# Performance work log

Hardware: AMD Instinct MI355X
Metric: run time of the kernel (lower is better)

## Reference

```python
import jax, jax.numpy as jnp
import numpy as np

NUM_NODES = 8192
IN_FEATURES = 1024
OUT_FEATURES = 512
NUM_EDGES = 262144  # avg degree 32


def setup_inputs() -> dict:
    key = jax.random.key(0)
    k_x, k_w, k_b, k_src, k_dst = jax.random.split(key, 5)
    x = jax.random.normal(k_x, (NUM_NODES, IN_FEATURES), dtype=jnp.float32)
    # torch nn.Linear layout: weight [out, in], bias [out]
    W = jax.random.normal(k_w, (OUT_FEATURES, IN_FEATURES), dtype=jnp.float32) * (1.0 / np.sqrt(IN_FEATURES))
    b = jax.random.normal(k_b, (OUT_FEATURES,), dtype=jnp.float32) * 0.01
    src = jax.random.randint(k_src, (NUM_EDGES,), 0, NUM_NODES, dtype=jnp.int64)
    dst = jax.random.randint(k_dst, (NUM_EDGES,), 0, NUM_NODES, dtype=jnp.int64)
    edge_index = jnp.stack([src, dst], axis=0)
    return {"x": x, "W": W, "b": b, "edge_index": edge_index, "num_nodes": NUM_NODES}


def reference(x, W, b, edge_index, num_nodes):
    # Faithful to the torch module: build dense adjacency from edge list
    # (duplicate edges collapse to 1.0 via assignment semantics),
    # linear, (dropout p=0 -> identity), dense adj @ hidden, relu.
    adj = jnp.zeros((num_nodes, num_nodes), dtype=x.dtype)
    adj = adj.at[edge_index[0], edge_index[1]].set(1.0)
    hidden = x @ W.T + b            # [N, out]
    support = adj @ hidden          # [N, out] aggregation over neighbors
    return jax.nn.relu(support)
```

## Files before the change

### kernel.cpp

```cpp
#include <hip/hip_runtime.h>

#define N_NODES 8192
#define IN_F    1024
#define OUT_F   512
#define N_EDGES 262144
#define STRIDE  96

#define HID_OFF     0u
#define XB_OFF      8388608u
#define WB_OFF      25165824u
#define DEG_OFF     26214400u
#define COL_OFF     26247168u
#define MAX_DEG     STRIDE

typedef short  bf16x8 __attribute__((ext_vector_type(8)));
typedef float  f32x4  __attribute__((ext_vector_type(4)));

__device__ __forceinline__ unsigned short f2bf(float f) {
    unsigned u = __float_as_uint(f);
    u += 0x7fffu + ((u >> 16) & 1u);
    return (unsigned short)(u >> 16);
}

__device__ __forceinline__ float bflo(unsigned u) { return __uint_as_float(u << 16); }
__device__ __forceinline__ float bfhi(unsigned u) { return __uint_as_float(u & 0xffff0000u); }

__device__ __forceinline__ void ld_lds16(const void* g, void* l) {
    __builtin_amdgcn_global_load_lds(
        (const __attribute__((address_space(1))) void*)g,
        (__attribute__((address_space(3))) void*)l, 16, 0, 0);
}

#define NX8 (N_NODES * IN_F / 8)
#define NW8 (OUT_F * IN_F / 8)
__global__ __launch_bounds__(256) void cvt_bf16_all(const float* __restrict__ x,
                                                    const float* __restrict__ w,
                                                    unsigned short* __restrict__ xb,
                                                    int* __restrict__ deg) {
    int i = blockIdx.x * blockDim.x + threadIdx.x;
    if (i < N_NODES) deg[i] = 0;
    if (i >= NX8 + NW8) return;
    const f32x4* p = (i < NX8) ? ((const f32x4*)x + (size_t)i * 2)
                               : ((const f32x4*)w + (size_t)(i - NX8) * 2);
    f32x4 v0 = __builtin_nontemporal_load(p);
    f32x4 v1 = __builtin_nontemporal_load(p + 1);
    uint4 o;
    o.x = (unsigned)f2bf(v0.x) | ((unsigned)f2bf(v0.y) << 16);
    o.y = (unsigned)f2bf(v0.z) | ((unsigned)f2bf(v0.w) << 16);
    o.z = (unsigned)f2bf(v1.x) | ((unsigned)f2bf(v1.y) << 16);
    o.w = (unsigned)f2bf(v1.z) | ((unsigned)f2bf(v1.w) << 16);
    *((uint4*)xb + i) = o;
}

__global__ __launch_bounds__(256, 6) void gemm_scatter(const unsigned short* __restrict__ Xb,
                                                       const unsigned short* __restrict__ Wb,
                                                       const float* __restrict__ bias,
                                                       unsigned short* __restrict__ H,
                                                       const int* __restrict__ src,
                                                       const int* __restrict__ dst,
                                                       int* __restrict__ deg,
                                                       int* __restrict__ col) {
    __shared__ unsigned short As[64 * 64];
    __shared__ unsigned short Bs[64 * 64];

    const int bid = blockIdx.x;
    const int tid = threadIdx.x;

    if (bid >= 1024) {
        int e = (bid - 1024) * 256 + tid;
        int s = src[e];
        int slot = atomicAdd(&deg[s], 1);
        if (slot < STRIDE) col[s * STRIDE + slot] = dst[e];
        return;
    }

    const int lane = tid & 63;
    const int wave = tid >> 6;
    const int row0 = (bid & 127) * 64;
    const int col0 = (bid >> 7) * 64;
    const int wm   = (wave & 1) * 32;
    const int wn   = (wave >> 1) * 32;
    const int fm   = lane & 15;
    const int fm7  = fm & 7;
    const int q    = lane >> 4;

    f32x4 acc[2][2];
#pragma unroll
    for (int i = 0; i < 2; ++i)
#pragma unroll
        for (int j = 0; j < 2; ++j) acc[i][j] = (f32x4)0.f;

    const int r0 = tid >> 3;
    const int kp = ((tid & 7) ^ (r0 & 7)) * 8;

    for (int k0 = 0; k0 < IN_F; k0 += 64) {
        ld_lds16(Xb + (size_t)(row0 + r0) * IN_F + k0 + kp,      As + tid * 8);
        ld_lds16(Xb + (size_t)(row0 + r0 + 32) * IN_F + k0 + kp, As + (tid + 256) * 8);
        ld_lds16(Wb + (size_t)(col0 + r0) * IN_F + k0 + kp,      Bs + tid * 8);
        ld_lds16(Wb + (size_t)(col0 + r0 + 32) * IN_F + k0 + kp, Bs + (tid + 256) * 8);
        __syncthreads();

#pragma unroll
        for (int s = 0; s < 2; ++s) {
            const int kq = s * 4 + q;
            bf16x8 a[2], b[2];
#pragma unroll
            for (int mi = 0; mi < 2; ++mi)
                a[mi] = *(const bf16x8*)&As[(((wm + mi * 16 + fm) << 3) + (kq ^ fm7)) << 3];
#pragma unroll
            for (int ni = 0; ni < 2; ++ni)
                b[ni] = *(const bf16x8*)&Bs[(((wn + ni * 16 + fm) << 3) + (kq ^ fm7)) << 3];
#pragma unroll
            for (int mi = 0; mi < 2; ++mi)
#pragma unroll
                for (int ni = 0; ni < 2; ++ni)
                    acc[mi][ni] = __builtin_amdgcn_mfma_f32_16x16x32_bf16(
                        a[mi], b[ni], acc[mi][ni], 0, 0, 0);
        }
        __syncthreads();
    }

    const int cm = (lane >> 4) * 4;
#pragma unroll
    for (int ni = 0; ni < 2; ++ni) {
        const int c = col0 + wn + ni * 16 + fm;
        const float bv = bias[c];
#pragma unroll
        for (int mi = 0; mi < 2; ++mi) {
#pragma unroll
            for (int r = 0; r < 4; ++r) {
                const int row = row0 + wm + mi * 16 + cm + r;
                H[(size_t)row * OUT_F + c] = f2bf(acc[mi][ni][r] + bv);
            }
        }
    }
}

__global__ __launch_bounds__(256) void aggregate(const unsigned short* __restrict__ H,
                                                 const int* __restrict__ dg,
                                                 const int* __restrict__ col,
                                                 float* __restrict__ out) {
    __shared__ int nbr[4][MAX_DEG];
    __shared__ int uniq[4][MAX_DEG];
    __shared__ int wcnt[4];
    const int wave = threadIdx.x >> 6;
    const int lane = threadIdx.x & 63;
    const int v    = blockIdx.x * 4 + wave;
    int d = dg[v];
    if (d > MAX_DEG) d = MAX_DEG;

    if (lane == 0) wcnt[wave] = 0;
    int id0 = -1, id1 = -1;
    if (lane < d)      { id0 = col[v * STRIDE + lane];      nbr[wave][lane]      = id0; }
    if (64 + lane < d) { id1 = col[v * STRIDE + 64 + lane]; nbr[wave][64 + lane] = id1; }
    __builtin_amdgcn_wave_barrier();

    bool k0 = (lane < d);
    const int lim0 = k0 ? lane : 0;
    for (int j = 0; j < lim0; ++j) k0 = k0 & (nbr[wave][j] != id0);
    bool k1 = (64 + lane < d);
    const int lim1 = k1 ? (64 + lane) : 0;
    for (int j = 0; j < lim1; ++j) k1 = k1 & (nbr[wave][j] != id1);
    if (k0) uniq[wave][atomicAdd(&wcnt[wave], 1)] = id0;
    if (k1) uniq[wave][atomicAdd(&wcnt[wave], 1)] = id1;
    __builtin_amdgcn_wave_barrier();
    const int n  = wcnt[wave];
    const int f0 = lane * 8;

    float a0=0,a1=0,a2=0,a3=0,a4=0,a5=0,a6=0,a7=0;
    int e = 0;
    for (; e + 4 <= n; e += 4) {
        const int i0 = uniq[wave][e], i1 = uniq[wave][e+1],
                  i2 = uniq[wave][e+2], i3 = uniq[wave][e+3];
        uint4 h0 = *(const uint4*)&H[(size_t)i0 * OUT_F + f0];
        uint4 h1 = *(const uint4*)&H[(size_t)i1 * OUT_F + f0];
        uint4 h2 = *(const uint4*)&H[(size_t)i2 * OUT_F + f0];
        uint4 h3 = *(const uint4*)&H[(size_t)i3 * OUT_F + f0];
        a0 += bflo(h0.x)+bflo(h1.x)+bflo(h2.x)+bflo(h3.x);
        a1 += bfhi(h0.x)+bfhi(h1.x)+bfhi(h2.x)+bfhi(h3.x);
        a2 += bflo(h0.y)+bflo(h1.y)+bflo(h2.y)+bflo(h3.y);
        a3 += bfhi(h0.y)+bfhi(h1.y)+bfhi(h2.y)+bfhi(h3.y);
        a4 += bflo(h0.z)+bflo(h1.z)+bflo(h2.z)+bflo(h3.z);
        a5 += bfhi(h0.z)+bfhi(h1.z)+bfhi(h2.z)+bfhi(h3.z);
        a6 += bflo(h0.w)+bflo(h1.w)+bflo(h2.w)+bflo(h3.w);
        a7 += bfhi(h0.w)+bfhi(h1.w)+bfhi(h2.w)+bfhi(h3.w);
    }
    for (; e < n; ++e) {
        uint4 h0 = *(const uint4*)&H[(size_t)uniq[wave][e] * OUT_F + f0];
        a0 += bflo(h0.x); a1 += bfhi(h0.x);
        a2 += bflo(h0.y); a3 += bfhi(h0.y);
        a4 += bflo(h0.z); a5 += bfhi(h0.z);
        a6 += bflo(h0.w); a7 += bfhi(h0.w);
    }
    f32x4 o0 = {fmaxf(a0,0.f), fmaxf(a1,0.f), fmaxf(a2,0.f), fmaxf(a3,0.f)};
    f32x4 o1 = {fmaxf(a4,0.f), fmaxf(a5,0.f), fmaxf(a6,0.f), fmaxf(a7,0.f)};
    __builtin_nontemporal_store(o0, (f32x4*)&out[(size_t)v * OUT_F + f0]);
    __builtin_nontemporal_store(o1, (f32x4*)&out[(size_t)v * OUT_F + f0 + 4]);
}

extern "C" void kernel_launch(void* const* d_in, const int* in_sizes, int n_in,
                              void* d_out, int out_size, void* d_ws, size_t ws_size,
                              hipStream_t stream) {
    const float* x  = (const float*)d_in[0];
    const float* W  = (const float*)d_in[1];
    const float* b  = (const float*)d_in[2];
    const int*   ei = (const int*)d_in[3];
    float* out = (float*)d_out;

    char* ws = (char*)d_ws;
    unsigned short* H   = (unsigned short*)(ws + HID_OFF);
    unsigned short* Xb  = (unsigned short*)(ws + XB_OFF);
    unsigned short* Wb  = (unsigned short*)(ws + WB_OFF);
    int*            deg = (int*)(ws + DEG_OFF);
    int*            col = (int*)(ws + COL_OFF);

    cvt_bf16_all<<<(NX8 + NW8 + 255) / 256, 256, 0, stream>>>(x, W, Xb, deg);

    gemm_scatter<<<2048, 256, 0, stream>>>(Xb, Wb, b, H, ei, ei + N_EDGES, deg, col);

    aggregate<<<N_NODES / 4, 256, 0, stream>>>(H, deg, col, out);
}
```

Before: 139.5 us.

## Double-buffer GEMM LDS with 128x64 tiles and unroll aggregation by eight

The GEMM tile grows from 64x64 to 128x64, cutting the grid to 512 GEMM blocks. Each wave now computes a 64x32 sub-tile, and the LDS stages are double-buffered so the next K-slice loads while MFMAs run on the current one. The aggregation loop gains an 8-way unrolled gather to keep more loads in flight. The trade-offs are more registers and LDS per block (launch bounds drop to 2) and fewer blocks, which may underfill the GPU.

```diff
diff --git a/kernel.cpp b/kernel.cpp
--- a/kernel.cpp
+++ b/kernel.cpp
@@ -52,7 +52,9 @@
     *((uint4*)xb + i) = o;
 }
 
-__global__ __launch_bounds__(256, 6) void gemm_scatter(const unsigned short* __restrict__ Xb,
+#define GEMM_BLOCKS 512
+
+__global__ __launch_bounds__(256, 2) void gemm_scatter(const unsigned short* __restrict__ Xb,
                                                        const unsigned short* __restrict__ Wb,
                                                        const float* __restrict__ bias,
                                                        unsigned short* __restrict__ H,
@@ -60,14 +62,14 @@
                                                        const int* __restrict__ dst,
                                                        int* __restrict__ deg,
                                                        int* __restrict__ col) {
-    __shared__ unsigned short As[64 * 64];
-    __shared__ unsigned short Bs[64 * 64];
+    __shared__ unsigned short As[2][128 * 64];
+    __shared__ unsigned short Bs[2][64 * 64];
 
     const int bid = blockIdx.x;
     const int tid = threadIdx.x;
 
-    if (bid >= 1024) {
-        int e = (bid - 1024) * 256 + tid;
+    if (bid >= GEMM_BLOCKS) {
+        int e = (bid - GEMM_BLOCKS) * 256 + tid;
         int s = src[e];
         int slot = atomicAdd(&deg[s], 1);
         if (slot < STRIDE) col[s * STRIDE + slot] = dst[e];
@@ -76,49 +78,64 @@
 
     const int lane = tid & 63;
     const int wave = tid >> 6;
-    const int row0 = (bid & 127) * 64;
-    const int col0 = (bid >> 7) * 64;
-    const int wm   = (wave & 1) * 32;
+    const int row0 = (bid & 63) * 128;
+    const int col0 = (bid >> 6) * 64;
+    const int wm   = (wave & 1) * 64;
     const int wn   = (wave >> 1) * 32;
     const int fm   = lane & 15;
     const int fm7  = fm & 7;
     const int q    = lane >> 4;
 
-    f32x4 acc[2][2];
-#pragma unroll
-    for (int i = 0; i < 2; ++i)
+    f32x4 acc[4][2];
+#pragma unroll
+    for (int i = 0; i < 4; ++i)
 #pragma unroll
         for (int j = 0; j < 2; ++j) acc[i][j] = (f32x4)0.f;
 
     const int r0 = tid >> 3;
     const int kp = ((tid & 7) ^ (r0 & 7)) * 8;
-
-    for (int k0 = 0; k0 < IN_F; k0 += 64) {
-        ld_lds16(Xb + (size_t)(row0 + r0) * IN_F + k0 + kp,      As + tid * 8);
-        ld_lds16(Xb + (size_t)(row0 + r0 + 32) * IN_F + k0 + kp, As + (tid + 256) * 8);
-        ld_lds16(Wb + (size_t)(col0 + r0) * IN_F + k0 + kp,      Bs + tid * 8);
-        ld_lds16(Wb + (size_t)(col0 + r0 + 32) * IN_F + k0 + kp, Bs + (tid + 256) * 8);
+    const unsigned short* Xbase = Xb + (size_t)(row0 + r0) * IN_F + kp;
+    const unsigned short* Wbase = Wb + (size_t)(col0 + r0) * IN_F + kp;
+
+#define STAGE(buf, k0) do {                                                   \
+    ld_lds16(Xbase            + (k0), &As[buf][tid * 8]);                     \
+    ld_lds16(Xbase + 32*IN_F  + (k0), &As[buf][(tid + 256) * 8]);             \
+    ld_lds16(Xbase + 64*IN_F  + (k0), &As[buf][(tid + 512) * 8]);             \
+    ld_lds16(Xbase + 96*IN_F  + (k0), &As[buf][(tid + 768) * 8]);             \
+    ld_lds16(Wbase            + (k0), &Bs[buf][tid * 8]);                     \
+    ld_lds16(Wbase + 32*IN_F  + (k0), &Bs[buf][(tid + 256) * 8]);             \
+} while (0)
+
+#define COMPUTE(buf) do {                                                     \
+    _Pragma("unroll")                                                         \
+    for (int s = 0; s < 2; ++s) {                                             \
+        const int kq = s * 4 + q;                                             \
+        bf16x8 a[4], b[2];                                                    \
+        _Pragma("unroll")                                                     \
+        for (int mi = 0; mi < 4; ++mi)                                        \
+            a[mi] = *(const bf16x8*)&As[buf][(((wm + mi*16 + fm) << 3) + (kq ^ fm7)) << 3]; \
+        _Pragma("unroll")                                                     \
+        for (int ni = 0; ni < 2; ++ni)                                        \
+            b[ni] = *(const bf16x8*)&Bs[buf][(((wn + ni*16 + fm) << 3) + (kq ^ fm7)) << 3]; \
+        _Pragma("unroll")                                                     \
+        for (int mi = 0; mi < 4; ++mi)                                        \
+            _Pragma("unroll")                                                 \
+            for (int ni = 0; ni < 2; ++ni)                                    \
+                acc[mi][ni] = __builtin_amdgcn_mfma_f32_16x16x32_bf16(        \
+                    a[mi], b[ni], acc[mi][ni], 0, 0, 0);                      \
+    }                                                                         \
+} while (0)
+
+    STAGE(0, 0);
+    __syncthreads();
+    int cur = 0;
+    for (int t = 0; t < 15; ++t) {
+        STAGE(cur ^ 1, (t + 1) * 64);
+        COMPUTE(cur);
         __syncthreads();
-
-#pragma unroll
-        for (int s = 0; s < 2; ++s) {
-            const int kq = s * 4 + q;
-            bf16x8 a[2], b[2];
-#pragma unroll
-            for (int mi = 0; mi < 2; ++mi)
-                a[mi] = *(const bf16x8*)&As[(((wm + mi * 16 + fm) << 3) + (kq ^ fm7)) << 3];
-#pragma unroll
-            for (int ni = 0; ni < 2; ++ni)
-                b[ni] = *(const bf16x8*)&Bs[(((wn + ni * 16 + fm) << 3) + (kq ^ fm7)) << 3];
-#pragma unroll
-            for (int mi = 0; mi < 2; ++mi)
-#pragma unroll
-                for (int ni = 0; ni < 2; ++ni)
-                    acc[mi][ni] = __builtin_amdgcn_mfma_f32_16x16x32_bf16(
-                        a[mi], b[ni], acc[mi][ni], 0, 0, 0);
-        }
-        __syncthreads();
-    }
+        cur ^= 1;
+    }
+    COMPUTE(cur);
 
     const int cm = (lane >> 4) * 4;
 #pragma unroll
@@ -126,7 +143,7 @@
         const int c = col0 + wn + ni * 16 + fm;
         const float bv = bias[c];
 #pragma unroll
-        for (int mi = 0; mi < 2; ++mi) {
+        for (int mi = 0; mi < 4; ++mi) {
 #pragma unroll
             for (int r = 0; r < 4; ++r) {
                 const int row = row0 + wm + mi * 16 + cm + r;
@@ -134,6 +151,8 @@
             }
         }
     }
+#undef STAGE
+#undef COMPUTE
 }
 
 __global__ __launch_bounds__(256) void aggregate(const unsigned short* __restrict__ H,
@@ -169,6 +188,36 @@
 
     float a0=0,a1=0,a2=0,a3=0,a4=0,a5=0,a6=0,a7=0;
     int e = 0;
+    for (; e + 8 <= n; e += 8) {
+        const int i0 = uniq[wave][e],   i1 = uniq[wave][e+1],
+                  i2 = uniq[wave][e+2], i3 = uniq[wave][e+3],
+                  i4 = uniq[wave][e+4], i5 = uniq[wave][e+5],
+                  i6 = uniq[wave][e+6], i7 = uniq[wave][e+7];
+        uint4 h0 = *(const uint4*)&H[(size_t)i0 * OUT_F + f0];
+        uint4 h1 = *(const uint4*)&H[(size_t)i1 * OUT_F + f0];
+        uint4 h2 = *(const uint4*)&H[(size_t)i2 * OUT_F + f0];
+        uint4 h3 = *(const uint4*)&H[(size_t)i3 * OUT_F + f0];
+        uint4 h4 = *(const uint4*)&H[(size_t)i4 * OUT_F + f0];
+        uint4 h5 = *(const uint4*)&H[(size_t)i5 * OUT_F + f0];
+        uint4 h6 = *(const uint4*)&H[(size_t)i6 * OUT_F + f0];
+        uint4 h7 = *(const uint4*)&H[(size_t)i7 * OUT_F + f0];
+        a0 += (bflo(h0.x)+bflo(h1.x)) + (bflo(h2.x)+bflo(h3.x))
+            + (bflo(h4.x)+bflo(h5.x)) + (bflo(h6.x)+bflo(h7.x));
+        a1 += (bfhi(h0.x)+bfhi(h1.x)) + (bfhi(h2.x)+bfhi(h3.x))
+            + (bfhi(h4.x)+bfhi(h5.x)) + (bfhi(h6.x)+bfhi(h7.x));
+        a2 += (bflo(h0.y)+bflo(h1.y)) + (bflo(h2.y)+bflo(h3.y))
+            + (bflo(h4.y)+bflo(h5.y)) + (bflo(h6.y)+bflo(h7.y));
+        a3 += (bfhi(h0.y)+bfhi(h1.y)) + (bfhi(h2.y)+bfhi(h3.y))
+            + (bfhi(h4.y)+bfhi(h5.y)) + (bfhi(h6.y)+bfhi(h7.y));
+        a4 += (bflo(h0.z)+bflo(h1.z)) + (bflo(h2.z)+bflo(h3.z))
+            + (bflo(h4.z)+bflo(h5.z)) + (bflo(h6.z)+bflo(h7.z));
+        a5 += (bfhi(h0.z)+bfhi(h1.z)) + (bfhi(h2.z)+bfhi(h3.z))
+            + (bfhi(h4.z)+bfhi(h5.z)) + (bfhi(h6.z)+bfhi(h7.z));
+        a6 += (bflo(h0.w)+bflo(h1.w)) + (bflo(h2.w)+bflo(h3.w))
+            + (bflo(h4.w)+bflo(h5.w)) + (bflo(h6.w)+bflo(h7.w));
+        a7 += (bfhi(h0.w)+bfhi(h1.w)) + (bfhi(h2.w)+bfhi(h3.w))
+            + (bfhi(h4.w)+bfhi(h5.w)) + (bfhi(h6.w)+bfhi(h7.w));
+    }
     for (; e + 4 <= n; e += 4) {
         const int i0 = uniq[wave][e], i1 = uniq[wave][e+1],
                   i2 = uniq[wave][e+2], i3 = uniq[wave][e+3];
@@ -216,7 +265,7 @@
 
     cvt_bf16_all<<<(NX8 + NW8 + 255) / 256, 256, 0, stream>>>(x, W, Xb, deg);
 
-    gemm_scatter<<<2048, 256, 0, stream>>>(Xb, Wb, b, H, ei, ei + N_EDGES, deg, col);
+    gemm_scatter<<<GEMM_BLOCKS + N_EDGES / 256, 256, 0, stream>>>(Xb, Wb, b, H, ei, ei + N_EDGES, deg, col);
 
     aggregate<<<N_NODES / 4, 256, 0, stream>>>(H, deg, col, out);
 }
```

Result: no change. 139.6 us (+0.1%).
